# Performance work log

Hardware: AMD Instinct MI355X
Metric: run time of the kernel (lower is better)

Reference implementation:

```python
import jax, jax.numpy as jnp
import numpy as np

B, T = 2048, 512
IN, H1, H2, D1 = 1, 128, 64, 25


def _lstm_layer(x, w_ih, w_hh, b_ih, b_hh):
    """PyTorch-style LSTM layer. x: [B,T,in], returns hidden seq [B,T,H].
    Gate order (PyTorch): i, f, g, o."""
    Bb = x.shape[0]
    H = w_hh.shape[1]
    # Precompute input projections for all timesteps: [B,T,4H]
    x_proj = jnp.einsum('bti,gi->btg', x, w_ih) + b_ih + b_hh

    def step(carry, xt):
        h, c = carry  # [B,H] each
        gates = xt + h @ w_hh.T  # [B,4H]
        i, f, g, o = jnp.split(gates, 4, axis=-1)
        i = jax.nn.sigmoid(i)
        f = jax.nn.sigmoid(f)
        g = jnp.tanh(g)
        o = jax.nn.sigmoid(o)
        c = f * c + i * g
        h = o * jnp.tanh(c)
        return (h, c), h

    h0 = jnp.zeros((Bb, H), x.dtype)
    c0 = jnp.zeros((Bb, H), x.dtype)
    (_, _), hs = jax.lax.scan(step, (h0, c0), jnp.swapaxes(x_proj, 0, 1))
    return jnp.swapaxes(hs, 0, 1)  # [B,T,H]


def setup_inputs() -> dict:
    key = jax.random.key(0)
    ks = jax.random.split(key, 13)
    s1 = 1.0 / np.sqrt(H1)
    s2 = 1.0 / np.sqrt(H2)
    sd1 = 1.0 / np.sqrt(H2)
    sd2 = 1.0 / np.sqrt(D1)
    u = lambda k, shape, s: jax.random.uniform(k, shape, jnp.float32, -s, s)
    return {
        'x': jax.random.normal(ks[0], (B, T, IN), jnp.float32),
        'w_ih1': u(ks[1], (4 * H1, IN), s1),
        'w_hh1': u(ks[2], (4 * H1, H1), s1),
        'b_ih1': u(ks[3], (4 * H1,), s1),
        'b_hh1': u(ks[4], (4 * H1,), s1),
        'w_ih2': u(ks[5], (4 * H2, H1), s2),
        'w_hh2': u(ks[6], (4 * H2, H2), s2),
        'b_ih2': u(ks[7], (4 * H2,), s2),
        'b_hh2': u(ks[8], (4 * H2,), s2),
        'w_d1': u(ks[9], (D1, H2), sd1),
        'b_d1': u(ks[10], (D1,), sd1),
        'w_d2': u(ks[11], (1, D1), sd2),
        'b_d2': u(ks[12], (1,), sd2),
    }


def reference(x, w_ih1, w_hh1, b_ih1, b_hh1, w_ih2, w_hh2, b_ih2, b_hh2,
              w_d1, b_d1, w_d2, b_d2):
    out = _lstm_layer(x, w_ih1, w_hh1, b_ih1, b_hh1)   # [B,T,128]
    out = _lstm_layer(out, w_ih2, w_hh2, b_ih2, b_hh2)  # [B,T,64]
    last = out[:, -1, :]                                 # [B,64]
    h = last @ w_d1.T + b_d1                             # [B,25]
    y = h @ w_d2.T + b_d2                                # [B,1]
    return y
```

## Files before the change

kernel.cpp:

```cpp
#include <hip/hip_runtime.h>

#define TS 512
#define LOG2E 1.4426950408889634f

typedef _Float16 f16x8 __attribute__((ext_vector_type(8)));
typedef float f32x4 __attribute__((ext_vector_type(4)));
typedef unsigned int u32;

#define MFMA16(a, b, c) __builtin_amdgcn_mfma_f32_16x16x32_f16((a), (b), (c), 0, 0, 0)

__global__ __launch_bounds__(512) void prep(
    const float* __restrict__ w_hh1, const float* __restrict__ w_ih1,
    const float* __restrict__ b_ih1, const float* __restrict__ b_hh1,
    const float* __restrict__ w_ih2, const float* __restrict__ w_hh2,
    _Float16* __restrict__ wsh)
{
  int idx = blockIdx.x * 512 + threadIdx.x;
  int l = (idx >> 3) & 63, j = idx & 7;
  float v;
  if (idx < 65536) {
    int f = idx >> 9;
    int wi = f >> 4, g = (f >> 2) & 3, kt = f & 3;
    int n = g * 128 + wi * 16 + (l & 15);
    int k = kt * 32 + (l >> 4) * 8 + j;
    v = w_hh1[n * 128 + k];
  } else if (idx < 81920) {
    int f = (idx - 65536) >> 9;
    int wi = f >> 2, g = f & 3;
    int n = g * 128 + wi * 16 + (l & 15);
    int s = (l >> 4) * 8 + j;
    v = (s == 0) ? (b_ih1[n] + b_hh1[n]) : ((s == 1) ? w_ih1[n] : 0.0f);
  } else {
    int f = (idx - 81920) >> 9;
    int w2 = f / 24, rem = f % 24, g = rem / 6, kt = rem % 6;
    int n = g * 64 + w2 * 16 + (l & 15);
    int k = kt * 32 + (l >> 4) * 8 + j;
    v = (k < 128) ? w_ih2[n * 128 + k] : w_hh2[n * 64 + (k - 128)];
  }
  wsh[idx] = (_Float16)(v * LOG2E);
}

__device__ __forceinline__ float rcpf_(float x) { return __builtin_amdgcn_rcpf(x); }
__device__ __forceinline__ float sig_s(float s)  { return rcpf_(1.0f + exp2f(-s)); }
__device__ __forceinline__ float tanh_s(float s) { return 1.0f - 2.0f * rcpf_(exp2f(s + s) + 1.0f); }
__device__ __forceinline__ float tanh_c(float c) { return 1.0f - 2.0f * rcpf_(exp2f(c * (2.0f * LOG2E)) + 1.0f); }


#define L1_BODY(I, PI, PIM)                                                    \
  {                                                                            \
    union { u32 uu[4]; f16x8 vv; } a6u;                                        \
    a6u.uu[0] = xpk[xrow + (I)];                                               \
    a6u.uu[1] = 0u; a6u.uu[2] = 0u; a6u.uu[3] = 0u;                            \
    f32x4 acc[4];                                                              \
    _Pragma("unroll") for (int g = 0; g < 4; ++g)                              \
      acc[g] = MFMA16(a6u.vv, BF[16 + g], zq);                                 \
    _Pragma("unroll") for (int kt = 0; kt < 4; ++kt) {                         \
      f16x8 av = *(const f16x8*)((PIM) + lofs + kt * 1024);                    \
      _Pragma("unroll") for (int g = 0; g < 4; ++g)                            \
        acc[g] = MFMA16(av, BF[g * 4 + kt], acc[g]);                           \
    }                                                                          \
    _Pragma("unroll") for (int rr = 0; rr < 2; ++rr) {                         \
      float sv[4];                                                             \
      _Pragma("unroll") for (int g = 0; g < 4; ++g) {                          \
        const float oth = __shfl_xor(acc[g][2 + rr], 32, 64);                  \
        sv[g] = up ? oth : acc[g][rr];                                         \
      }                                                                        \
      const float ii = sig_s(sv[0]), ff = sig_s(sv[1]);                        \
      const float gv = tanh_s(sv[2]), oo = sig_s(sv[3]);                       \
      cst[rr] = fmaf(ff, cst[rr], ii * gv);                                    \
      const float hv = oo * tanh_c(cst[rr]);                                   \
      *(_Float16*)((PI) + ha[rr]) = (_Float16)hv;                              \
    }                                                                          \
  }

#define L2_BODY(PI, PIM, WRLDS, WRF)                                           \
  {                                                                            \
    f32x4 acc[4];                                                              \
    {                                                                          \
      f16x8 ev = *(const f16x8*)((PIM) + lofs);                                \
      _Pragma("unroll") for (int g = 0; g < 4; ++g)                            \
        acc[g] = MFMA16(ev, BF[g * 6], zq);                                    \
    }                                                                          \
    _Pragma("unroll") for (int kt = 1; kt < 4; ++kt) {                         \
      f16x8 ev = *(const f16x8*)((PIM) + lofs + kt * 1024);                    \
      _Pragma("unroll") for (int g = 0; g < 4; ++g)                            \
        acc[g] = MFMA16(ev, BF[g * 6 + kt], acc[g]);                           \
    }                                                                          \
    _Pragma("unroll") for (int kt = 4; kt < 6; ++kt) {                         \
      f16x8 ev = *(const f16x8*)((PI) + lofs + kt * 1024);                     \
      _Pragma("unroll") for (int g = 0; g < 4; ++g)                            \
        acc[g] = MFMA16(ev, BF[g * 6 + kt], acc[g]);                           \
    }                                                                          \
    _Pragma("unroll") for (int rr = 0; rr < 2; ++rr) {                         \
      float sv[4];                                                             \
      _Pragma("unroll") for (int g = 0; g < 4; ++g) {                          \
        const float oth = __shfl_xor(acc[g][2 + rr], 32, 64);                  \
        sv[g] = (up ? oth : acc[g][rr]) + biv[g];                              \
      }                                                                        \
      const float ii = sig_s(sv[0]), ff = sig_s(sv[1]);                        \
      const float gv = tanh_s(sv[2]), oo = sig_s(sv[3]);                       \
      cst[rr] = fmaf(ff, cst[rr], ii * gv);                                    \
      const float hv = oo * tanh_c(cst[rr]);                                   \
      if (WRLDS) *(_Float16*)((PIM) + ha[rr]) = (_Float16)hv;                  \
      if (WRF) h2f[rb + rr][u2] = hv;                                          \
    }                                                                          \
  }

__global__ __launch_bounds__(768, 3) void lstm_mfma(
    const float* __restrict__ x,
    const float* __restrict__ b_ih2, const float* __restrict__ b_hh2,
    const float* __restrict__ w_d1, const float* __restrict__ b_d1,
    const float* __restrict__ w_d2, const float* __restrict__ b_d2,
    const _Float16* __restrict__ wsh,
    float* __restrict__ out)
{
  __shared__ __align__(16) _Float16 HC[2 * 3072];
  __shared__ __align__(16) u32 xpk[8 * 516];
  __shared__ float h2f[8][65];
  __shared__ float dh[200];

  const int tid = threadIdx.x;
  const int w   = tid >> 6;
  const int l   = tid & 63;
  const int col = l & 15;
  const int q   = l >> 4;
  const int up  = q >> 1;
  const int rb  = 4 * (q & 1) + 2 * up;
  const int wg  = (w < 8) ? 0 : 1;
  const int w2  = w - 8;
  const int r0  = blockIdx.x * 8;
  const int lofs = l * 16;
  const int xrow = (l & 7) * 516;
  const int u2  = (wg == 1) ? (w2 * 16 + col) : 0;

  f16x8 BF[24];
  float biv[4] = {0.f, 0.f, 0.f, 0.f};
  int ha[2];

  if (wg == 0) {
    #pragma unroll
    for (int f = 0; f < 16; ++f)
      BF[f] = *(const f16x8*)(wsh + (w * 16 + f) * 512 + l * 8);
    #pragma unroll
    for (int g = 0; g < 4; ++g)
      BF[16 + g] = *(const f16x8*)(wsh + 65536 + (w * 4 + g) * 512 + l * 8);
    const int u = w * 16 + col;
    #pragma unroll
    for (int rr = 0; rr < 2; ++rr)
      ha[rr] = (u >> 5) * 1024 + ((rb + rr) + ((u >> 3) & 3) * 16) * 16 + (u & 7) * 2;
  } else {
    #pragma unroll
    for (int f = 0; f < 24; ++f)
      BF[f] = *(const f16x8*)(wsh + 81920 + (w2 * 24 + f) * 512 + l * 8);
    #pragma unroll
    for (int g = 0; g < 4; ++g)
      biv[g] = (b_ih2[g * 64 + u2] + b_hh2[g * 64 + u2]) * LOG2E;
    #pragma unroll
    for (int rr = 0; rr < 2; ++rr)
      ha[rr] = (4 + (u2 >> 5)) * 1024 + ((rb + rr) + ((u2 >> 3) & 3) * 16) * 16 + (u2 & 7) * 2;
  }

  for (int i = tid; i < 4096; i += 768) {
    int r = i >> 9, t = i & 511;
    union { _Float16 h; unsigned short s; } cv;
    cv.h = (_Float16)x[(r0 + r) * 512 + t];
    xpk[r * 516 + t] = 0x3C00u | ((u32)cv.s << 16);
  }
  for (int i = tid; i < 3072; i += 768) ((u32*)HC)[i] = 0u;

  float cst[2] = {0.f, 0.f};
  const f32x4 zq = {0.f, 0.f, 0.f, 0.f};
  char* const hcb = (char*)HC;
  __syncthreads();

  #pragma unroll 1
  for (int i = 0; i < TS; i += 2) {
    if (wg == 0)      { L1_BODY(i, hcb, hcb + 6144) }
    else if (i > 0)   { L2_BODY(hcb, hcb + 6144, 1, 0) }
    __syncthreads();
    if (wg == 0)      { L1_BODY(i + 1, hcb + 6144, hcb) }
    else              { L2_BODY(hcb + 6144, hcb, 1, 0) }
    __syncthreads();
  }
  if (wg == 1)        { L2_BODY(hcb, hcb + 6144, 0, 1) }
  __syncthreads();

  if (tid < 200) {
    int r = tid / 25, d = tid - r * 25;
    float acc = b_d1[d];
    #pragma unroll
    for (int uu = 0; uu < 64; ++uu) acc = fmaf(h2f[r][uu], w_d1[d * 64 + uu], acc);
    dh[tid] = acc;
  }
  __syncthreads();
  if (tid < 8) {
    float y = b_d2[0];
    #pragma unroll
    for (int d = 0; d < 25; ++d) y = fmaf(dh[tid * 25 + d], w_d2[d], y);
    out[r0 + tid] = y;
  }
}

extern "C" void kernel_launch(void* const* d_in, const int* in_sizes, int n_in,
                              void* d_out, int out_size, void* d_ws, size_t ws_size,
                              hipStream_t stream) {
  (void)in_sizes; (void)n_in; (void)out_size; (void)ws_size;
  const float* x     = (const float*)d_in[0];
  const float* w_ih1 = (const float*)d_in[1];
  const float* w_hh1 = (const float*)d_in[2];
  const float* b_ih1 = (const float*)d_in[3];
  const float* b_hh1 = (const float*)d_in[4];
  const float* w_ih2 = (const float*)d_in[5];
  const float* w_hh2 = (const float*)d_in[6];
  const float* b_ih2 = (const float*)d_in[7];
  const float* b_hh2 = (const float*)d_in[8];
  const float* w_d1  = (const float*)d_in[9];
  const float* b_d1  = (const float*)d_in[10];
  const float* w_d2  = (const float*)d_in[11];
  const float* b_d2  = (const float*)d_in[12];
  _Float16* wsh = (_Float16*)d_ws;
  float* outp = (float*)d_out;

  prep<<<256, 512, 0, stream>>>(w_hh1, w_ih1, b_ih1, b_hh1, w_ih2, w_hh2, wsh);
  lstm_mfma<<<256, 768, 0, stream>>>(x, b_ih2, b_hh2, w_d1, b_d1, w_d2, b_d2, wsh, outp);
}
```

Baseline: 573.8 us.

## Batch LDS loads before MFMA chains, skip padded rows, merge gate reciprocals

All A-operand LDS loads for each step are now issued up front, and only lanes holding valid batch rows (col<8) load them; the other lanes feed zeros. The MFMA chain is reordered per gate and wrapped in s_setprio to favour matrix issue. The gate epilogue merges sigmoid(i)*tanh(g) and sigmoid(o)*tanh(c) into a single reciprocal each, with a clamp on the cell exponent to avoid overflow. This cuts LDS traffic and transcendental/rcp count on the serial recurrence path, but the serialized per-gate accumulation changes MFMA dependency patterns.

```diff
diff --git a/kernel.cpp b/kernel.cpp
--- a/kernel.cpp
+++ b/kernel.cpp
@@ -41,66 +41,82 @@
 }
 
 __device__ __forceinline__ float rcpf_(float x) { return __builtin_amdgcn_rcpf(x); }
-__device__ __forceinline__ float sig_s(float s)  { return rcpf_(1.0f + exp2f(-s)); }
-__device__ __forceinline__ float tanh_s(float s) { return 1.0f - 2.0f * rcpf_(exp2f(s + s) + 1.0f); }
-__device__ __forceinline__ float tanh_c(float c) { return 1.0f - 2.0f * rcpf_(exp2f(c * (2.0f * LOG2E)) + 1.0f); }
-
+
+
+#define EPILOGUE(RR, HV)                                                       \
+      const float e0 = exp2f(-sv[0]);                                          \
+      const float E2 = exp2f(sv[2] + sv[2]);                                   \
+      const float ig = (E2 - 1.0f) * rcpf_((1.0f + e0) * (E2 + 1.0f));         \
+      const float ff = rcpf_(1.0f + exp2f(-sv[1]));                            \
+      cst[RR] = fmaf(ff, cst[RR], ig);                                         \
+      const float tc = fminf(cst[RR] * (2.0f * LOG2E), 120.0f);                \
+      const float Ec = exp2f(tc);                                              \
+      const float e3 = exp2f(-sv[3]);                                          \
+      const float HV = (Ec - 1.0f) * rcpf_((1.0f + e3) * (Ec + 1.0f));
 
 #define L1_BODY(I, PI, PIM)                                                    \
   {                                                                            \
     union { u32 uu[4]; f16x8 vv; } a6u;                                        \
     a6u.uu[0] = xpk[xrow + (I)];                                               \
     a6u.uu[1] = 0u; a6u.uu[2] = 0u; a6u.uu[3] = 0u;                            \
+    f16x8 a0 = (f16x8){0,0,0,0,0,0,0,0}, a1 = a0, a2 = a0, a3 = a0;            \
+    if (mrow) {                                                                \
+      a0 = *(const f16x8*)((PIM) + lofs);                                      \
+      a1 = *(const f16x8*)((PIM) + lofs + 1024);                               \
+      a2 = *(const f16x8*)((PIM) + lofs + 2048);                               \
+      a3 = *(const f16x8*)((PIM) + lofs + 3072);                               \
+    }                                                                          \
+    __builtin_amdgcn_s_setprio(1);                                             \
     f32x4 acc[4];                                                              \
-    _Pragma("unroll") for (int g = 0; g < 4; ++g)                              \
+    _Pragma("unroll") for (int g = 0; g < 4; ++g) {                            \
       acc[g] = MFMA16(a6u.vv, BF[16 + g], zq);                                 \
-    _Pragma("unroll") for (int kt = 0; kt < 4; ++kt) {                         \
-      f16x8 av = *(const f16x8*)((PIM) + lofs + kt * 1024);                    \
-      _Pragma("unroll") for (int g = 0; g < 4; ++g)                            \
-        acc[g] = MFMA16(av, BF[g * 4 + kt], acc[g]);                           \
-    }                                                                          \
+      acc[g] = MFMA16(a0, BF[g * 4 + 0], acc[g]);                              \
+      acc[g] = MFMA16(a1, BF[g * 4 + 1], acc[g]);                              \
+      acc[g] = MFMA16(a2, BF[g * 4 + 2], acc[g]);                              \
+      acc[g] = MFMA16(a3, BF[g * 4 + 3], acc[g]);                              \
+    }                                                                          \
+    __builtin_amdgcn_s_setprio(0);                                             \
     _Pragma("unroll") for (int rr = 0; rr < 2; ++rr) {                         \
       float sv[4];                                                             \
       _Pragma("unroll") for (int g = 0; g < 4; ++g) {                          \
         const float oth = __shfl_xor(acc[g][2 + rr], 32, 64);                  \
         sv[g] = up ? oth : acc[g][rr];                                         \
       }                                                                        \
-      const float ii = sig_s(sv[0]), ff = sig_s(sv[1]);                        \
-      const float gv = tanh_s(sv[2]), oo = sig_s(sv[3]);                       \
-      cst[rr] = fmaf(ff, cst[rr], ii * gv);                                    \
-      const float hv = oo * tanh_c(cst[rr]);                                   \
+      EPILOGUE(rr, hv)                                                         \
       *(_Float16*)((PI) + ha[rr]) = (_Float16)hv;                              \
     }                                                                          \
   }
 
 #define L2_BODY(PI, PIM, WRLDS, WRF)                                           \
   {                                                                            \
+    f16x8 e0v = (f16x8){0,0,0,0,0,0,0,0}, e1v = e0v, e2v = e0v, e3v = e0v,     \
+          e4v = e0v, e5v = e0v;                                                \
+    if (mrow) {                                                                \
+      e0v = *(const f16x8*)((PIM) + lofs);                                     \
+      e1v = *(const f16x8*)((PIM) + lofs + 1024);                              \
+      e2v = *(const f16x8*)((PIM) + lofs + 2048);                              \
+      e3v = *(const f16x8*)((PIM) + lofs + 3072);                              \
+      e4v = *(const f16x8*)((PI) + lofs + 4096);                               \
+      e5v = *(const f16x8*)((PI) + lofs + 5120);                               \
+    }                                                                          \
+    __builtin_amdgcn_s_setprio(1);                                             \
     f32x4 acc[4];                                                              \
-    {                                                                          \
-      f16x8 ev = *(const f16x8*)((PIM) + lofs);                                \
-      _Pragma("unroll") for (int g = 0; g < 4; ++g)                            \
-        acc[g] = MFMA16(ev, BF[g * 6], zq);                                    \
-    }                                                                          \
-    _Pragma("unroll") for (int kt = 1; kt < 4; ++kt) {                         \
-      f16x8 ev = *(const f16x8*)((PIM) + lofs + kt * 1024);                    \
-      _Pragma("unroll") for (int g = 0; g < 4; ++g)                            \
-        acc[g] = MFMA16(ev, BF[g * 6 + kt], acc[g]);                           \
-    }                                                                          \
-    _Pragma("unroll") for (int kt = 4; kt < 6; ++kt) {                         \
-      f16x8 ev = *(const f16x8*)((PI) + lofs + kt * 1024);                     \
-      _Pragma("unroll") for (int g = 0; g < 4; ++g)                            \
-        acc[g] = MFMA16(ev, BF[g * 6 + kt], acc[g]);                           \
-    }                                                                          \
+    _Pragma("unroll") for (int g = 0; g < 4; ++g) {                            \
+      acc[g] = MFMA16(e0v, BF[g * 6 + 0], zq);                                 \
+      acc[g] = MFMA16(e1v, BF[g * 6 + 1], acc[g]);                             \
+      acc[g] = MFMA16(e2v, BF[g * 6 + 2], acc[g]);                             \
+      acc[g] = MFMA16(e3v, BF[g * 6 + 3], acc[g]);                             \
+      acc[g] = MFMA16(e4v, BF[g * 6 + 4], acc[g]);                             \
+      acc[g] = MFMA16(e5v, BF[g * 6 + 5], acc[g]);                             \
+    }                                                                          \
+    __builtin_amdgcn_s_setprio(0);                                             \
     _Pragma("unroll") for (int rr = 0; rr < 2; ++rr) {                         \
       float sv[4];                                                             \
       _Pragma("unroll") for (int g = 0; g < 4; ++g) {                          \
         const float oth = __shfl_xor(acc[g][2 + rr], 32, 64);                  \
         sv[g] = (up ? oth : acc[g][rr]) + biv[g];                              \
       }                                                                        \
-      const float ii = sig_s(sv[0]), ff = sig_s(sv[1]);                        \
-      const float gv = tanh_s(sv[2]), oo = sig_s(sv[3]);                       \
-      cst[rr] = fmaf(ff, cst[rr], ii * gv);                                    \
-      const float hv = oo * tanh_c(cst[rr]);                                   \
+      EPILOGUE(rr, hv)                                                         \
       if (WRLDS) *(_Float16*)((PIM) + ha[rr]) = (_Float16)hv;                  \
       if (WRF) h2f[rb + rr][u2] = hv;                                          \
     }                                                                          \
@@ -131,6 +147,7 @@
   const int r0  = blockIdx.x * 8;
   const int lofs = l * 16;
   const int xrow = (l & 7) * 516;
+  const bool mrow = (l & 15) < 8;
   const int u2  = (wg == 1) ? (w2 * 16 + col) : 0;
 
   f16x8 BF[24];
```

Result: slower. 630.4 us (+9.9%).
